# Kernel optimization log

Hardware: AMD Instinct MI355X
Metric: run time of the kernel (lower is better)

The kernel has to match this reference:

```python
import jax, jax.numpy as jnp
import numpy as np

HIDDEN = 768
HEADS = 12
HEAD_DIM = HIDDEN // HEADS


def setup_inputs() -> dict:
    key = jax.random.key(0)
    ks = jax.random.split(key, 6)
    B, N = 32, 577  # N = 1 CLS + 576 patches
    x = jax.random.normal(ks[0], (B, N, HIDDEN), dtype=jnp.float32)
    seg_bias = jax.random.uniform(ks[1], (B, N - 1), dtype=jnp.float32)
    w_qkv = jax.random.normal(ks[2], (HIDDEN, 3 * HIDDEN), dtype=jnp.float32) * 0.02
    b_qkv = jnp.zeros((3 * HIDDEN,), dtype=jnp.float32)
    w_proj = jax.random.normal(ks[3], (HIDDEN, HIDDEN), dtype=jnp.float32) * 0.02
    b_proj = jnp.zeros((HIDDEN,), dtype=jnp.float32)
    seg_scale = jnp.ones((), dtype=jnp.float32)
    return {"x": x, "seg_bias": seg_bias, "w_qkv": w_qkv, "b_qkv": b_qkv,
            "w_proj": w_proj, "b_proj": b_proj, "seg_scale": seg_scale}


def reference(x, seg_bias, w_qkv, b_qkv, w_proj, b_proj, seg_scale):
    B, N, _ = x.shape
    scale = HEAD_DIM ** -0.5
    qkv = x @ w_qkv + b_qkv                       # (B, N, 3*H*D)
    qkv = qkv.reshape(B, N, 3, HEADS, HEAD_DIM)
    q = qkv[:, :, 0].transpose(0, 2, 1, 3)        # (B, H, N, D)
    k = qkv[:, :, 1].transpose(0, 2, 1, 3)
    v = qkv[:, :, 2].transpose(0, 2, 1, 3)
    attn = jnp.einsum('bhqd,bhkd->bhqk', q, k) * scale  # (B, H, N, N)
    # additive seg bias on CLS-query row, patch keys only (cols 1:)
    bias = (seg_bias * seg_scale)[:, None, None, :]     # (B,1,1,N-1)
    attn = attn.at[:, :, 0:1, 1:].add(bias)
    attn = jax.nn.softmax(attn, axis=-1)
    out = jnp.einsum('bhqk,bhkd->bhqd', attn, v)        # (B, H, N, D)
    out = out.transpose(0, 2, 1, 3).reshape(B, N, HIDDEN)
    return out @ w_proj + b_proj
```

## Files before the change

### kernel.cpp

```cpp
#include <hip/hip_runtime.h>


typedef unsigned short bf16_t;
typedef __attribute__((ext_vector_type(8))) short short8;
typedef __attribute__((ext_vector_type(4))) float f32x4;

#define B_    32
#define N_    577
#define BN_   18464
#define HID_  768
#define NH_   12
#define HD_   64
#define QKVC_ 2304
#define NPAD_ 640

__device__ __forceinline__ bf16_t f2bf(float f) {
  union { float f; unsigned u; } x; x.f = f;
  unsigned r = x.u + 0x7fffu + ((x.u >> 16) & 1u);
  return (bf16_t)(r >> 16);
}

__global__ __launch_bounds__(256) void cast_kernel(const float* __restrict__ in,
                                                   bf16_t* __restrict__ out, int n4) {
  int i = blockIdx.x * 256 + threadIdx.x;
  if (i >= n4) return;
  float4 v = ((const float4*)in)[i];
  ushort4 o;
  o.x = f2bf(v.x); o.y = f2bf(v.y); o.z = f2bf(v.z); o.w = f2bf(v.w);
  ((ushort4*)out)[i] = o;
}

__global__ __launch_bounds__(256) void transpose_cast_kernel(const float* __restrict__ in,
                                                             bf16_t* __restrict__ out,
                                                             int R, int C) {
  __shared__ float tile[32][33];
  int c0 = blockIdx.x * 32, r0 = blockIdx.y * 32;
  int tx = threadIdx.x, ty = threadIdx.y;
  #pragma unroll
  for (int i = ty; i < 32; i += 8)
    tile[i][tx] = in[(size_t)(r0 + i) * C + c0 + tx];
  __syncthreads();
  #pragma unroll
  for (int i = ty; i < 32; i += 8)
    out[(size_t)(c0 + i) * R + r0 + tx] = f2bf(tile[tx][i]);
}

template <int OUT_BF16>
__global__ __launch_bounds__(256, 3) void gemm_bf16_kernel(
    const bf16_t* __restrict__ A,
    const bf16_t* __restrict__ Bt,
    const float* __restrict__ bias,
    void* __restrict__ Cout,
    int M, int Nc) {
  __shared__ bf16_t As[128 * 64];
  __shared__ bf16_t Bs[128 * 64];

  const int tid  = threadIdx.x;
  const int lane = tid & 63, w = tid >> 6;
  const int quad = lane >> 4, l16 = lane & 15;

  const int Mb = (M + 127) >> 7;
  const int Nb = Nc >> 7;
  const int np_full = Mb >> 3;
  const int rem = Mb - np_full * 8;
  int bid = blockIdx.x;
  int m_blk, n_blk;
  int body = np_full * 8 * Nb;
  if (bid < body) {
    int p = bid / (8 * Nb), local = bid % (8 * Nb);
    m_blk = p * 8 + (local & 7);
    n_blk = local >> 3;
  } else {
    int t = bid - body;
    m_blk = np_full * 8 + t % rem;
    n_blk = t / rem;
  }
  const int m0 = m_blk * 128, n0 = n_blk * 128;
  const int wm = (w >> 1) * 64, wn = (w & 1) * 64;

  f32x4 acc[4][4];
  #pragma unroll
  for (int i = 0; i < 4; ++i)
    #pragma unroll
    for (int j = 0; j < 4; ++j)
      acc[i][j] = (f32x4){0.f, 0.f, 0.f, 0.f};

  for (int kt = 0; kt < 768; kt += 64) {
    __syncthreads();
    #pragma unroll
    for (int it = 0; it < 4; ++it) {
      int gi = it * 256 + tid;
      int row = gi >> 3, chp = gi & 7;
      int ch = chp ^ (row & 7);
      int gm = m0 + row; if (gm >= M) gm = M - 1;
      __builtin_amdgcn_global_load_lds(
          (const __attribute__((address_space(1))) unsigned int*)(A + (size_t)gm * 768 + kt + ch * 8),
          (__attribute__((address_space(3))) unsigned int*)(As + gi * 8),
          16, 0, 0);
      int gn = n0 + row;
      __builtin_amdgcn_global_load_lds(
          (const __attribute__((address_space(1))) unsigned int*)(Bt + (size_t)gn * 768 + kt + ch * 8),
          (__attribute__((address_space(3))) unsigned int*)(Bs + gi * 8),
          16, 0, 0);
    }
    __syncthreads();

    #pragma unroll
    for (int ks = 0; ks < 2; ++ks) {
      short8 af[4], bfr[4];
      #pragma unroll
      for (int i = 0; i < 4; ++i) {
        int row = wm + i * 16 + l16;
        int c = ks * 4 + quad;
        af[i] = *(const short8*)(As + row * 64 + (c ^ (row & 7)) * 8);
      }
      #pragma unroll
      for (int j = 0; j < 4; ++j) {
        int row = wn + j * 16 + l16;
        int c = ks * 4 + quad;
        bfr[j] = *(const short8*)(Bs + row * 64 + (c ^ (row & 7)) * 8);
      }
      #pragma unroll
      for (int i = 0; i < 4; ++i)
        #pragma unroll
        for (int j = 0; j < 4; ++j)
          acc[i][j] = __builtin_amdgcn_mfma_f32_16x16x32_bf16(af[i], bfr[j], acc[i][j], 0, 0, 0);
    }
  }

  #pragma unroll
  for (int i = 0; i < 4; ++i) {
    int mrow_base = m0 + wm + i * 16 + quad * 4;
    #pragma unroll
    for (int j = 0; j < 4; ++j) {
      int col = n0 + wn + j * 16 + l16;
      float bs = bias[col];
      #pragma unroll
      for (int r = 0; r < 4; ++r) {
        int row = mrow_base + r;
        if (row < M) {
          float v = acc[i][j][r] + bs;
          if (OUT_BF16)
            ((bf16_t*)Cout)[(size_t)row * Nc + col] = f2bf(v);
          else
            ((float*)Cout)[(size_t)row * Nc + col] = v;
        }
      }
    }
  }
}

__global__ __launch_bounds__(256) void vt_kernel(const bf16_t* __restrict__ qkv,
                                                 bf16_t* __restrict__ vT) {
  const int t = blockIdx.x, h = blockIdx.y, b = blockIdx.z;
  const int tid = threadIdx.x;
  __shared__ bf16_t Ls[64 * 65];
  const int kv0 = t * 64;
  const bf16_t* Vp = qkv + (size_t)b * N_ * QKVC_ + 2 * HID_ + h * HD_;

  #pragma unroll
  for (int it = 0; it < 2; ++it) {
    int idx = it * 256 + tid;
    int row = idx >> 3, ch = idx & 7;
    int krow = kv0 + row; if (krow > N_ - 1) krow = N_ - 1;
    short8 v8 = *(const short8*)(Vp + (size_t)krow * QKVC_ + ch * 8);
    #pragma unroll
    for (int j = 0; j < 8; ++j)
      Ls[(ch * 8 + j) * 65 + row] = (bf16_t)v8[j];
  }
  __syncthreads();
  bf16_t* outp = vT + ((size_t)(b * NH_ + h) * HD_) * NPAD_;
  #pragma unroll
  for (int it = 0; it < 2; ++it) {
    int idx = it * 256 + tid;
    int d = idx >> 3, kc = idx & 7;
    short8 o8;
    #pragma unroll
    for (int j = 0; j < 8; ++j)
      o8[j] = (short)Ls[d * 65 + kc * 8 + j];
    *(short8*)(outp + (size_t)d * NPAD_ + kv0 + kc * 8) = o8;
  }
}

__global__ __launch_bounds__(256) void attn_kernel(
    const bf16_t* __restrict__ qkv,
    const bf16_t* __restrict__ vT,
    const float* __restrict__ seg_bias,
    const float* __restrict__ seg_scale,
    bf16_t* __restrict__ out) {
  const int qt = blockIdx.x;
  const int h  = blockIdx.y;
  const int b  = blockIdx.z;
  const int tid = threadIdx.x;
  const int w = tid >> 6, lane = tid & 63;
  const int quad = lane >> 4, l16 = lane & 15;

  __shared__ bf16_t Ks[64 * 72];
  __shared__ bf16_t Vt[64 * 72];
  __shared__ bf16_t Pb[4][32 * 72];

  const bf16_t* Qbase = qkv + (size_t)b * N_ * QKVC_ + h * HD_;
  const bf16_t* Kbase = Qbase + HID_;
  const bf16_t* Vtb   = vT + ((size_t)(b * NH_ + h) * HD_) * NPAD_;

  const int q0 = qt * 128 + w * 32;
  short8 qf[2][2];
  #pragma unroll
  for (int mi = 0; mi < 2; ++mi) {
    int qr = q0 + mi * 16 + l16;
    if (qr > N_ - 1) qr = N_ - 1;
    qf[mi][0] = *(const short8*)(Qbase + (size_t)qr * QKVC_ + quad * 8);
    qf[mi][1] = *(const short8*)(Qbase + (size_t)qr * QKVC_ + 32 + quad * 8);
  }

  f32x4 o[2][4];
  float lsum[2][4];
  #pragma unroll
  for (int mi = 0; mi < 2; ++mi)
    #pragma unroll
    for (int j = 0; j < 4; ++j) {
      o[mi][j] = (f32x4){0.f, 0.f, 0.f, 0.f};
      lsum[mi][j] = 0.f;
    }

  const float ss = seg_scale[0] * 1.44269504f;
  const bool bias_wave = (qt == 0 && w == 0);
  bf16_t* pw = Pb[w];

  for (int t = 0; t < 10; ++t) {
    const int kv0 = t * 64;
    __syncthreads();
    #pragma unroll
    for (int it = 0; it < 2; ++it) {
      int idx = it * 256 + tid;
      int row = idx >> 3, ch = idx & 7;
      int krow = kv0 + row; if (krow > N_ - 1) krow = N_ - 1;
      short8 k8 = *(const short8*)(Kbase + (size_t)krow * QKVC_ + ch * 8);
      *(short8*)(Ks + row * 72 + ch * 8) = k8;
      short8 v8 = *(const short8*)(Vtb + (size_t)row * NPAD_ + kv0 + ch * 8);
      *(short8*)(Vt + row * 72 + ch * 8) = v8;
    }
    __syncthreads();

    f32x4 s[2][4];
    #pragma unroll
    for (int mi = 0; mi < 2; ++mi)
      #pragma unroll
      for (int sub = 0; sub < 4; ++sub)
        s[mi][sub] = (f32x4){0.f, 0.f, 0.f, 0.f};
    #pragma unroll
    for (int sub = 0; sub < 4; ++sub) {
      short8 k0 = *(const short8*)(Ks + (sub * 16 + l16) * 72 + quad * 8);
      short8 k1 = *(const short8*)(Ks + (sub * 16 + l16) * 72 + 32 + quad * 8);
      #pragma unroll
      for (int mi = 0; mi < 2; ++mi) {
        s[mi][sub] = __builtin_amdgcn_mfma_f32_16x16x32_bf16(qf[mi][0], k0, s[mi][sub], 0, 0, 0);
        s[mi][sub] = __builtin_amdgcn_mfma_f32_16x16x32_bf16(qf[mi][1], k1, s[mi][sub], 0, 0, 0);
      }
    }

    #pragma unroll
    for (int mi = 0; mi < 2; ++mi)
      #pragma unroll
      for (int sub = 0; sub < 4; ++sub) {
        int key = kv0 + sub * 16 + l16;
        #pragma unroll
        for (int r = 0; r < 4; ++r) {
          float v = s[mi][sub][r] * 0.180336881f;
          if (bias_wave && mi == 0 && quad == 0 && r == 0 && key >= 1 && key < N_)
            v += seg_bias[b * (N_ - 1) + key - 1] * ss;
          float p = exp2f(v);
          if (key >= N_) p = 0.f;
          lsum[mi][r] += p;
          pw[(mi * 16 + quad * 4 + r) * 72 + sub * 16 + l16] = f2bf(p);
        }
      }

    #pragma unroll
    for (int mi = 0; mi < 2; ++mi) {
      short8 pa0 = *(const short8*)(pw + (mi * 16 + l16) * 72 + quad * 8);
      short8 pa1 = *(const short8*)(pw + (mi * 16 + l16) * 72 + 32 + quad * 8);
      #pragma unroll
      for (int ds = 0; ds < 4; ++ds) {
        short8 vb0 = *(const short8*)(Vt + (ds * 16 + l16) * 72 + quad * 8);
        short8 vb1 = *(const short8*)(Vt + (ds * 16 + l16) * 72 + 32 + quad * 8);
        o[mi][ds] = __builtin_amdgcn_mfma_f32_16x16x32_bf16(pa0, vb0, o[mi][ds], 0, 0, 0);
        o[mi][ds] = __builtin_amdgcn_mfma_f32_16x16x32_bf16(pa1, vb1, o[mi][ds], 0, 0, 0);
      }
    }
  }

  #pragma unroll
  for (int mi = 0; mi < 2; ++mi)
    #pragma unroll
    for (int r = 0; r < 4; ++r) {
      float l = lsum[mi][r];
      #pragma unroll
      for (int off = 1; off < 16; off <<= 1)
        l += __shfl_xor(l, off);
      float inv = 1.0f / l;
      int row = q0 + mi * 16 + quad * 4 + r;
      if (row < N_) {
        size_t base = ((size_t)b * N_ + row) * HID_ + h * HD_;
        #pragma unroll
        for (int ds = 0; ds < 4; ++ds)
          out[base + ds * 16 + l16] = f2bf(o[mi][ds][r] * inv);
      }
    }
}

extern "C" void kernel_launch(void* const* d_in, const int* in_sizes, int n_in,
                              void* d_out, int out_size, void* d_ws, size_t ws_size,
                              hipStream_t stream) {
  const float* x         = (const float*)d_in[0];
  const float* seg_bias  = (const float*)d_in[1];
  const float* w_qkv     = (const float*)d_in[2];
  const float* b_qkv     = (const float*)d_in[3];
  const float* w_proj    = (const float*)d_in[4];
  const float* b_proj    = (const float*)d_in[5];
  const float* seg_scale = (const float*)d_in[6];

  char* ws = (char*)d_ws;
  bf16_t* xb     = (bf16_t*)ws;
  bf16_t* wqkvT  = (bf16_t*)(ws + 28360704);
  bf16_t* wprojT = (bf16_t*)(ws + 31899648);
  bf16_t* qkvb   = (bf16_t*)(ws + 33079296);
  bf16_t* vT     = (bf16_t*)(ws + 118161408);
  bf16_t* attnb  = xb;

  cast_kernel<<<(BN_ * HID_ / 4) / 256, 256, 0, stream>>>(x, xb, BN_ * HID_ / 4);
  dim3 tb(32, 8);
  transpose_cast_kernel<<<dim3(QKVC_ / 32, HID_ / 32), tb, 0, stream>>>(w_qkv, wqkvT, HID_, QKVC_);
  transpose_cast_kernel<<<dim3(HID_ / 32, HID_ / 32), tb, 0, stream>>>(w_proj, wprojT, HID_, HID_);

  gemm_bf16_kernel<1><<<145 * (QKVC_ / 128), 256, 0, stream>>>(
      xb, wqkvT, b_qkv, (void*)qkvb, BN_, QKVC_);

  vt_kernel<<<dim3(10, NH_, B_), 256, 0, stream>>>(qkvb, vT);

  attn_kernel<<<dim3(5, NH_, B_), 256, 0, stream>>>(qkvb, vT, seg_bias, seg_scale, attnb);

  gemm_bf16_kernel<0><<<145 * (HID_ / 128), 256, 0, stream>>>(
      attnb, wprojT, b_proj, d_out, BN_, HID_);
}
```

Measured before the change: 353.0 us.

## Double-buffer K/V tiles in attention and fold softmax scale into Q

The attention kernel now double-buffers its K and V shared-memory tiles. The next tile is loaded into registers while the current one is computed, and one barrier per iteration replaces two. The softmax scale is folded into Q up front, so the per-element multiply is gone; the bias add is hoisted out of the softmax loop and key masking only runs on the last tile. Other changes: a cheaper round-to-nearest bf16 conversion, a transposed P layout in LDS, and a 1D grid ordered so query tiles of the same (batch, head) are spread apart. The risks are higher LDS and register use, which may lower occupancy, and slightly different rounding from scaling Q in bf16.

```diff
diff --git a/kernel.cpp b/kernel.cpp
--- a/kernel.cpp
+++ b/kernel.cpp
@@ -188,15 +188,17 @@
     const float* __restrict__ seg_bias,
     const float* __restrict__ seg_scale,
     bf16_t* __restrict__ out) {
-  const int qt = blockIdx.x;
-  const int h  = blockIdx.y;
-  const int b  = blockIdx.z;
+  const int bid  = blockIdx.x;
+  const int pair = bid % (B_ * NH_);
+  const int qt   = bid / (B_ * NH_);
+  const int h    = pair % NH_;
+  const int b    = pair / NH_;
   const int tid = threadIdx.x;
   const int w = tid >> 6, lane = tid & 63;
   const int quad = lane >> 4, l16 = lane & 15;
 
-  __shared__ bf16_t Ks[64 * 72];
-  __shared__ bf16_t Vt[64 * 72];
+  __shared__ bf16_t Ks[2][64 * 72];
+  __shared__ bf16_t Vt[2][64 * 72];
   __shared__ bf16_t Pb[4][32 * 72];
 
   const bf16_t* Qbase = qkv + (size_t)b * N_ * QKVC_ + h * HD_;
@@ -212,6 +214,17 @@
     qf[mi][0] = *(const short8*)(Qbase + (size_t)qr * QKVC_ + quad * 8);
     qf[mi][1] = *(const short8*)(Qbase + (size_t)qr * QKVC_ + 32 + quad * 8);
   }
+  const float qsc = 0.125f * 1.44269504f;
+  #pragma unroll
+  for (int mi = 0; mi < 2; ++mi)
+    #pragma unroll
+    for (int c = 0; c < 2; ++c)
+      #pragma unroll
+      for (int j = 0; j < 8; ++j) {
+        unsigned u = ((unsigned)(unsigned short)qf[mi][c][j]) << 16;
+        union { unsigned u; float f; } x; x.u = u;
+        qf[mi][c][j] = (short)f2bf(x.f * qsc);
+      }
 
   f32x4 o[2][4];
   float lsum[2][4];
@@ -223,24 +236,45 @@
       lsum[mi][j] = 0.f;
     }
 
-  const float ss = seg_scale[0] * 1.44269504f;
+  const float ssl = seg_scale[0] * 1.44269504f;
   const bool bias_wave = (qt == 0 && w == 0);
   bf16_t* pw = Pb[w];
 
+  const int srow = tid >> 3;
+  const int sch  = tid & 7;
+
+  short8 kpre[2], vpre[2];
+  #pragma unroll
+  for (int it = 0; it < 2; ++it) {
+    int row = it * 32 + srow;
+    int krow = row; if (krow > N_ - 1) krow = N_ - 1;
+    kpre[it] = *(const short8*)(Kbase + (size_t)krow * QKVC_ + sch * 8);
+    vpre[it] = *(const short8*)(Vtb + (size_t)row * NPAD_ + sch * 8);
+  }
+  #pragma unroll
+  for (int it = 0; it < 2; ++it) {
+    int row = it * 32 + srow;
+    *(short8*)(&Ks[0][0] + row * 72 + sch * 8) = kpre[it];
+    *(short8*)(&Vt[0][0] + row * 72 + sch * 8) = vpre[it];
+  }
+  __syncthreads();
+
   for (int t = 0; t < 10; ++t) {
+    const int cur = t & 1;
     const int kv0 = t * 64;
-    __syncthreads();
-    #pragma unroll
-    for (int it = 0; it < 2; ++it) {
-      int idx = it * 256 + tid;
-      int row = idx >> 3, ch = idx & 7;
-      int krow = kv0 + row; if (krow > N_ - 1) krow = N_ - 1;
-      short8 k8 = *(const short8*)(Kbase + (size_t)krow * QKVC_ + ch * 8);
-      *(short8*)(Ks + row * 72 + ch * 8) = k8;
-      short8 v8 = *(const short8*)(Vtb + (size_t)row * NPAD_ + kv0 + ch * 8);
-      *(short8*)(Vt + row * 72 + ch * 8) = v8;
-    }
-    __syncthreads();
+    const bf16_t* ks = &Ks[cur][0];
+    const bf16_t* vt = &Vt[cur][0];
+
+    if (t < 9) {
+      const int kv1 = kv0 + 64;
+      #pragma unroll
+      for (int it = 0; it < 2; ++it) {
+        int row = it * 32 + srow;
+        int krow = kv1 + row; if (krow > N_ - 1) krow = N_ - 1;
+        kpre[it] = *(const short8*)(Kbase + (size_t)krow * QKVC_ + sch * 8);
+        vpre[it] = *(const short8*)(Vtb + (size_t)row * NPAD_ + kv1 + sch * 8);
+      }
+    }
 
     f32x4 s[2][4];
     #pragma unroll
@@ -250,8 +284,8 @@
         s[mi][sub] = (f32x4){0.f, 0.f, 0.f, 0.f};
     #pragma unroll
     for (int sub = 0; sub < 4; ++sub) {
-      short8 k0 = *(const short8*)(Ks + (sub * 16 + l16) * 72 + quad * 8);
-      short8 k1 = *(const short8*)(Ks + (sub * 16 + l16) * 72 + 32 + quad * 8);
+      short8 k0 = *(const short8*)(ks + (sub * 16 + l16) * 72 + quad * 8);
+      short8 k1 = *(const short8*)(ks + (sub * 16 + l16) * 72 + 32 + quad * 8);
       #pragma unroll
       for (int mi = 0; mi < 2; ++mi) {
         s[mi][sub] = __builtin_amdgcn_mfma_f32_16x16x32_bf16(qf[mi][0], k0, s[mi][sub], 0, 0, 0);
@@ -259,35 +293,58 @@
       }
     }
 
-    #pragma unroll
-    for (int mi = 0; mi < 2; ++mi)
+    if (bias_wave && quad == 0) {
       #pragma unroll
       for (int sub = 0; sub < 4; ++sub) {
         int key = kv0 + sub * 16 + l16;
+        if (key >= 1 && key < N_)
+          s[0][sub][0] += seg_bias[b * (N_ - 1) + key - 1] * ssl;
+      }
+    }
+
+    #pragma unroll
+    for (int mi = 0; mi < 2; ++mi)
+      #pragma unroll
+      for (int sub = 0; sub < 4; ++sub) {
         #pragma unroll
         for (int r = 0; r < 4; ++r) {
-          float v = s[mi][sub][r] * 0.180336881f;
-          if (bias_wave && mi == 0 && quad == 0 && r == 0 && key >= 1 && key < N_)
-            v += seg_bias[b * (N_ - 1) + key - 1] * ss;
-          float p = exp2f(v);
-          if (key >= N_) p = 0.f;
+          float p = exp2f(s[mi][sub][r]);
+          if (t == 9) {
+            int key = kv0 + sub * 16 + l16;
+            if (key >= N_) p = 0.f;
+          }
           lsum[mi][r] += p;
-          pw[(mi * 16 + quad * 4 + r) * 72 + sub * 16 + l16] = f2bf(p);
+          union { float f; unsigned u; } c; c.f = p;
+          pw[(mi * 16 + r * 4 + quad) * 72 + sub * 16 + l16] =
+              (bf16_t)((c.u + 0x8000u) >> 16);
         }
       }
 
     #pragma unroll
     for (int mi = 0; mi < 2; ++mi) {
-      short8 pa0 = *(const short8*)(pw + (mi * 16 + l16) * 72 + quad * 8);
-      short8 pa1 = *(const short8*)(pw + (mi * 16 + l16) * 72 + 32 + quad * 8);
+      int prow = mi * 16 + ((l16 & 3) << 2) + (l16 >> 2);
+      short8 pa0 = *(const short8*)(pw + prow * 72 + quad * 8);
+      short8 pa1 = *(const short8*)(pw + prow * 72 + 32 + quad * 8);
       #pragma unroll
       for (int ds = 0; ds < 4; ++ds) {
-        short8 vb0 = *(const short8*)(Vt + (ds * 16 + l16) * 72 + quad * 8);
-        short8 vb1 = *(const short8*)(Vt + (ds * 16 + l16) * 72 + 32 + quad * 8);
+        short8 vb0 = *(const short8*)(vt + (ds * 16 + l16) * 72 + quad * 8);
+        short8 vb1 = *(const short8*)(vt + (ds * 16 + l16) * 72 + 32 + quad * 8);
         o[mi][ds] = __builtin_amdgcn_mfma_f32_16x16x32_bf16(pa0, vb0, o[mi][ds], 0, 0, 0);
         o[mi][ds] = __builtin_amdgcn_mfma_f32_16x16x32_bf16(pa1, vb1, o[mi][ds], 0, 0, 0);
       }
     }
+
+    if (t < 9) {
+      bf16_t* ksn = &Ks[1 - cur][0];
+      bf16_t* vtn = &Vt[1 - cur][0];
+      #pragma unroll
+      for (int it = 0; it < 2; ++it) {
+        int row = it * 32 + srow;
+        *(short8*)(ksn + row * 72 + sch * 8) = kpre[it];
+        *(short8*)(vtn + row * 72 + sch * 8) = vpre[it];
+      }
+    }
+    __syncthreads();
   }
 
   #pragma unroll
@@ -338,7 +395,7 @@
 
   vt_kernel<<<dim3(10, NH_, B_), 256, 0, stream>>>(qkvb, vT);
 
-  attn_kernel<<<dim3(5, NH_, B_), 256, 0, stream>>>(qkvb, vT, seg_bias, seg_scale, attnb);
+  attn_kernel<<<5 * NH_ * B_, 256, 0, stream>>>(qkvb, vT, seg_bias, seg_scale, attnb);
 
   gemm_bf16_kernel<0><<<145 * (HID_ / 128), 256, 0, stream>>>(
       attnb, wprojT, b_proj, d_out, BN_, HID_);
```

Result: faster. 342.1 us (-3.1%).
